# Performance work log

Measured on AMD Instinct MI355X. Metric: run time of the kernel, lower is better.

Reference implementation:

```python
import math
import jax, jax.numpy as jnp
import numpy as np

B, N, D = 16, 2048, 64

def setup_inputs() -> dict:
    key = jax.random.key(0)
    kq, kk, kv, kl = jax.random.split(key, 4)
    q = jax.random.normal(kq, (B, N, D), dtype=jnp.float32)
    k = jax.random.normal(kk, (B, N, D), dtype=jnp.float32)
    v = jax.random.normal(kv, (B, N, D), dtype=jnp.float32)
    valid = jax.random.randint(kl, (B, N), 0, 2048, dtype=jnp.int64 if jax.config.jax_enable_x64 else jnp.int32)
    return {"q": q, "k": k, "v": v, "valid": valid}

def reference(q, k, v, valid):
    # scores[b,i,j] = <q[b,i], k[b,j]> / sqrt(d)
    d = k.shape[-1]
    scores = jnp.einsum('bid,bjd->bij', q, k) / jnp.sqrt(jnp.asarray(d, q.dtype))
    # mask[b,i,j] = (j+1) > valid[b,i]; masked positions replaced by 1e-6
    # (faithful to torch.masked_fill(scores, mask, 1e-06) -- NOT -inf)
    key_pos = jnp.arange(1, scores.shape[-1] + 1)  # [N]
    mask = key_pos[None, None, :] > valid[:, :, None]  # [B,N,N]
    mask_scores = jnp.where(mask, jnp.asarray(1e-06, scores.dtype), scores)
    weights = jax.nn.softmax(mask_scores, axis=-1)
    # dropout p=0.0 -> identity
    return jnp.einsum('bij,bjd->bid', weights, v)
```

## Files before the change

kernel.cpp:

```cpp
#include <hip/hip_runtime.h>
#include <stdint.h>

#define BB 16
#define NN 2048
#define DD 64
#define BM 64
#define BN 64
#define KSTR 72
#define PSTR 72

typedef __attribute__((ext_vector_type(8))) short short8;
typedef __attribute__((ext_vector_type(4))) float f32x4;

__device__ __forceinline__ unsigned short f2bf(float f) {
  union { float f; uint32_t u; } c; c.f = f;
  uint32_t u = c.u + 0x7fffu + ((c.u >> 16) & 1u);
  return (unsigned short)(u >> 16);
}
__device__ __forceinline__ unsigned short f2bf_fast(float f) {
  union { float f; uint32_t u; } c; c.f = f;
  return (unsigned short)((c.u + 0x8000u) >> 16);
}

__global__ __launch_bounds__(256) void prep_kernel(const float* __restrict__ k,
                                                   const float* __restrict__ v,
                                                   unsigned short* __restrict__ kbf,
                                                   unsigned short* __restrict__ vt) {
  __shared__ float t[64][65];
  int id = blockIdx.x, tid = threadIdx.x;
  if (id < 2048) {
    int i = id * 256 + tid;
    float4 f = ((const float4*)k)[i];
    ushort4 o;
    o.x = f2bf(f.x); o.y = f2bf(f.y); o.z = f2bf(f.z); o.w = f2bf(f.w);
    ((ushort4*)kbf)[i] = o;
  } else {
    int bid = id - 2048;
    int b = bid >> 5;
    int k0 = (bid & 31) * 64;
    const float4* src = (const float4*)(v + ((size_t)b * NN + k0) * DD);
#pragma unroll
    for (int i = 0; i < 4; i++) {
      int f4 = tid + i * 256;
      int row = f4 >> 4, c4 = f4 & 15;
      float4 f = src[f4];
      t[row][c4*4+0] = f.x; t[row][c4*4+1] = f.y; t[row][c4*4+2] = f.z; t[row][c4*4+3] = f.w;
    }
    __syncthreads();
    int d = tid >> 2, kg = tid & 3;
    unsigned short* dst = vt + ((size_t)b * DD + d) * NN + k0 + kg * 16;
#pragma unroll
    for (int u = 0; u < 4; u++) {
      ushort4 o;
      o.x = f2bf(t[kg*16+u*4+0][d]);
      o.y = f2bf(t[kg*16+u*4+1][d]);
      o.z = f2bf(t[kg*16+u*4+2][d]);
      o.w = f2bf(t[kg*16+u*4+3][d]);
      ((ushort4*)dst)[u] = o;
    }
  }
}

__global__ __launch_bounds__(256, 4) void attn_kernel(
    const float* __restrict__ q, const unsigned short* __restrict__ kbf,
    const unsigned short* __restrict__ vtbf, const int* __restrict__ valid,
    float* __restrict__ out, unsigned short* __restrict__ po,
    float* __restrict__ pz, int nsplit)
{
  __shared__ __align__(16) unsigned short Klds[BN * KSTR];
  __shared__ __align__(16) unsigned short Vlds[DD * KSTR];
  __shared__ __align__(16) unsigned short Plds[4 * 16 * PSTR];
  __shared__ int vld[BM];

  int id = blockIdx.x;
  int x = id & 7, r = id >> 3;
  int b = x + 8 * (r & 1);
  int r2 = r >> 1;
  int sp, qt;
  if (nsplit == 2) { sp = r2 & 1; qt = r2 >> 1; }
  else             { sp = 0;      qt = r2;      }
  int i0 = qt * BM;
  int jbase = sp * (NN / nsplit);
  int jlen  = NN / nsplit;

  int tid = threadIdx.x;
  int w = tid >> 6;
  int lane = tid & 63;
  int m = lane & 15;
  int quad = lane >> 4;

  if (tid < BM) vld[tid] = valid[b * NN + i0 + tid];

  short8 qf[2];
  {
    const float* qp = q + ((size_t)b * NN + (i0 + w * 16 + m)) * DD;
#pragma unroll
    for (int s = 0; s < 2; s++) {
      float4 f0 = *(const float4*)(qp + s * 32 + quad * 8);
      float4 f1 = *(const float4*)(qp + s * 32 + quad * 8 + 4);
      union { short8 v; unsigned short u[8]; } tmp;
      tmp.u[0]=f2bf(f0.x*0.125f); tmp.u[1]=f2bf(f0.y*0.125f);
      tmp.u[2]=f2bf(f0.z*0.125f); tmp.u[3]=f2bf(f0.w*0.125f);
      tmp.u[4]=f2bf(f1.x*0.125f); tmp.u[5]=f2bf(f1.y*0.125f);
      tmp.u[6]=f2bf(f1.z*0.125f); tmp.u[7]=f2bf(f1.w*0.125f);
      qf[s] = tmp.v;
    }
  }

  __syncthreads();
  int vr[4];
#pragma unroll
  for (int rr = 0; rr < 4; rr++) vr[rr] = vld[w * 16 + quad * 4 + rr];

  f32x4 o[4] = {{0,0,0,0},{0,0,0,0},{0,0,0,0},{0,0,0,0}};
  float z[4] = {0,0,0,0};
  unsigned short* pbase = Plds + w * 16 * PSTR;

  int srow = tid >> 2, scol = (tid & 3) * 16;
  const unsigned short* gk = kbf + ((size_t)(b * NN + jbase + srow)) * DD + scol;
  const unsigned short* gv = vtbf + ((size_t)b * DD + srow) * NN + jbase + scol;

  uint4 ka = *(const uint4*)gk, kb2 = *(const uint4*)(gk + 8);
  uint4 va = *(const uint4*)gv, vb2 = *(const uint4*)(gv + 8);

  int iters = jlen / BN;
  for (int it = 0; it < iters; ++it) {
    int j0 = jbase + it * BN;
    __syncthreads();
    *(uint4*)&Klds[srow * KSTR + scol]     = ka;
    *(uint4*)&Klds[srow * KSTR + scol + 8] = kb2;
    *(uint4*)&Vlds[srow * KSTR + scol]     = va;
    *(uint4*)&Vlds[srow * KSTR + scol + 8] = vb2;
    if (it + 1 < iters) {
      gk += BN * DD; gv += BN;
      ka = *(const uint4*)gk; kb2 = *(const uint4*)(gk + 8);
      va = *(const uint4*)gv; vb2 = *(const uint4*)(gv + 8);
    }
    __syncthreads();

    f32x4 s[4] = {{0,0,0,0},{0,0,0,0},{0,0,0,0},{0,0,0,0}};
#pragma unroll
    for (int sub = 0; sub < 4; sub++) {
#pragma unroll
      for (int ss = 0; ss < 2; ss++) {
        short8 kf = *(const short8*)&Klds[(sub * 16 + m) * KSTR + ss * 32 + quad * 8];
        s[sub] = __builtin_amdgcn_mfma_f32_16x16x32_bf16(qf[ss], kf, s[sub], 0, 0, 0);
      }
    }

#pragma unroll
    for (int sub = 0; sub < 4; sub++) {
      int j = j0 + sub * 16 + m;
#pragma unroll
      for (int rr = 0; rr < 4; rr++) {
        float arg = (j < vr[rr]) ? s[sub][rr] : 1.0e-6f;
        float e = __expf(arg);
        z[rr] += e;
        pbase[(quad * 4 + rr) * PSTR + sub * 16 + m] = f2bf_fast(e);
      }
    }

    __builtin_amdgcn_s_waitcnt(0xc07f);

#pragma unroll
    for (int ss = 0; ss < 2; ss++) {
      short8 pf = *(const short8*)&pbase[m * PSTR + ss * 32 + quad * 8];
#pragma unroll
      for (int t = 0; t < 4; t++) {
        short8 vf = *(const short8*)&Vlds[(t * 16 + m) * KSTR + ss * 32 + quad * 8];
        o[t] = __builtin_amdgcn_mfma_f32_16x16x32_bf16(pf, vf, o[t], 0, 0, 0);
      }
    }
  }

  float zred[4];
#pragma unroll
  for (int rr = 0; rr < 4; rr++) {
    float zz = z[rr];
    zz += __shfl_xor(zz, 1, 16);
    zz += __shfl_xor(zz, 2, 16);
    zz += __shfl_xor(zz, 4, 16);
    zz += __shfl_xor(zz, 8, 16);
    zred[rr] = zz;
  }

  if (nsplit == 2) {
#pragma unroll
    for (int rr = 0; rr < 4; rr++) {
      int row = i0 + w * 16 + quad * 4 + rr;
      unsigned short* op = po + ((size_t)((sp * BB + b) * NN) + row) * DD + m;
#pragma unroll
      for (int t = 0; t < 4; t++) op[t * 16] = f2bf_fast(o[t][rr]);
      if (m == 0) pz[(size_t)(sp * BB + b) * NN + row] = zred[rr];
    }
  } else {
#pragma unroll
    for (int rr = 0; rr < 4; rr++) {
      float inv = 1.0f / zred[rr];
      int row = i0 + w * 16 + quad * 4 + rr;
      float* op = out + ((size_t)b * NN + row) * DD + m;
#pragma unroll
      for (int t = 0; t < 4; t++) op[t * 16] = o[t][rr] * inv;
    }
  }
}

__global__ __launch_bounds__(256) void combine_kernel(const unsigned short* __restrict__ po,
                                                      const float* __restrict__ pz,
                                                      float* __restrict__ out) {
  int gid = blockIdx.x * 256 + threadIdx.x;
  size_t base = (size_t)gid * 8;
  int rowz = gid >> 3;
  uint4 a = *(const uint4*)(po + base);
  uint4 c = *(const uint4*)(po + (size_t)BB * NN * DD + base);
  float inv = 1.0f / (pz[rowz] + pz[(size_t)BB * NN + rowz]);
  uint32_t aw[4] = {a.x, a.y, a.z, a.w}, cw[4] = {c.x, c.y, c.z, c.w};
  float r[8];
#pragma unroll
  for (int i = 0; i < 4; i++) {
    float alo = __uint_as_float(aw[i] << 16), ahi = __uint_as_float(aw[i] & 0xffff0000u);
    float clo = __uint_as_float(cw[i] << 16), chi = __uint_as_float(cw[i] & 0xffff0000u);
    r[2*i]   = (alo + clo) * inv;
    r[2*i+1] = (ahi + chi) * inv;
  }
  float4* op = (float4*)(out + base);
  op[0] = make_float4(r[0], r[1], r[2], r[3]);
  op[1] = make_float4(r[4], r[5], r[6], r[7]);
}

extern "C" void kernel_launch(void* const* d_in, const int* in_sizes, int n_in,
                              void* d_out, int out_size, void* d_ws, size_t ws_size,
                              hipStream_t stream) {
  const float* q = (const float*)d_in[0];
  const float* k = (const float*)d_in[1];
  const float* v = (const float*)d_in[2];
  const int* valid = (const int*)d_in[3];
  float* out = (float*)d_out;

  unsigned short* kbf  = (unsigned short*)d_ws;
  unsigned short* vtbf = kbf + (size_t)BB * NN * DD;
  unsigned short* po   = vtbf + (size_t)BB * NN * DD;
  float* pz = (float*)(po + (size_t)2 * BB * NN * DD);

  size_t need = (size_t)4 * BB * NN * DD * 2 + (size_t)2 * BB * NN * 4;
  int nsplit = (ws_size >= need) ? 2 : 1;

  hipLaunchKernelGGL(prep_kernel, dim3(2560), dim3(256), 0, stream, k, v, kbf, vtbf);
  hipLaunchKernelGGL(attn_kernel, dim3(512 * nsplit), dim3(256), 0, stream,
                     q, kbf, vtbf, valid, out, po, pz, nsplit);
  if (nsplit == 2)
    hipLaunchKernelGGL(combine_kernel, dim3(1024), dim3(256), 0, stream, po, pz, out);
}
```

Before: 117.2 us.

## Template split-K attention with 4-way key split and transposed MFMA operands

After: 115.8 us. No clear change (-1.2%).

```diff
diff --git a/kernel.cpp b/kernel.cpp
--- a/kernel.cpp
+++ b/kernel.cpp
@@ -1,4 +1,5 @@
 #include <hip/hip_runtime.h>
+#include <hip/hip_bf16.h>
 #include <stdint.h>
 
 #define BB 16
@@ -17,9 +18,10 @@
   uint32_t u = c.u + 0x7fffu + ((c.u >> 16) & 1u);
   return (unsigned short)(u >> 16);
 }
-__device__ __forceinline__ unsigned short f2bf_fast(float f) {
-  union { float f; uint32_t u; } c; c.f = f;
-  return (unsigned short)((c.u + 0x8000u) >> 16);
+__device__ __forceinline__ uint32_t pkrn(float a, float b) {
+  union { __hip_bfloat162 h; uint32_t u; } c;
+  c.h = __float22bfloat162_rn(make_float2(a, b));
+  return c.u;
 }
 
 __global__ __launch_bounds__(256) void prep_kernel(const float* __restrict__ k,
@@ -61,27 +63,28 @@
   }
 }
 
+template <int NS>
 __global__ __launch_bounds__(256, 4) void attn_kernel(
     const float* __restrict__ q, const unsigned short* __restrict__ kbf,
     const unsigned short* __restrict__ vtbf, const int* __restrict__ valid,
     float* __restrict__ out, unsigned short* __restrict__ po,
-    float* __restrict__ pz, int nsplit)
+    float* __restrict__ pz)
 {
+  constexpr int JLEN = NN / NS;
+  constexpr int ITERS = JLEN / BN;
+
   __shared__ __align__(16) unsigned short Klds[BN * KSTR];
   __shared__ __align__(16) unsigned short Vlds[DD * KSTR];
   __shared__ __align__(16) unsigned short Plds[4 * 16 * PSTR];
   __shared__ int vld[BM];
 
   int id = blockIdx.x;
-  int x = id & 7, r = id >> 3;
-  int b = x + 8 * (r & 1);
-  int r2 = r >> 1;
-  int sp, qt;
-  if (nsplit == 2) { sp = r2 & 1; qt = r2 >> 1; }
-  else             { sp = 0;      qt = r2;      }
+  int b = (id & 7) + 8 * ((id >> 3) & 1);
+  int rest = id >> 4;
+  int sp = rest % NS;
+  int qt = rest / NS;
   int i0 = qt * BM;
-  int jbase = sp * (NN / nsplit);
-  int jlen  = NN / nsplit;
+  int jbase = sp * JLEN;
 
   int tid = threadIdx.x;
   int w = tid >> 6;
@@ -98,22 +101,20 @@
     for (int s = 0; s < 2; s++) {
       float4 f0 = *(const float4*)(qp + s * 32 + quad * 8);
       float4 f1 = *(const float4*)(qp + s * 32 + quad * 8 + 4);
-      union { short8 v; unsigned short u[8]; } tmp;
-      tmp.u[0]=f2bf(f0.x*0.125f); tmp.u[1]=f2bf(f0.y*0.125f);
-      tmp.u[2]=f2bf(f0.z*0.125f); tmp.u[3]=f2bf(f0.w*0.125f);
-      tmp.u[4]=f2bf(f1.x*0.125f); tmp.u[5]=f2bf(f1.y*0.125f);
-      tmp.u[6]=f2bf(f1.z*0.125f); tmp.u[7]=f2bf(f1.w*0.125f);
+      union { short8 v; uint32_t x[4]; } tmp;
+      tmp.x[0] = pkrn(f0.x * 0.125f, f0.y * 0.125f);
+      tmp.x[1] = pkrn(f0.z * 0.125f, f0.w * 0.125f);
+      tmp.x[2] = pkrn(f1.x * 0.125f, f1.y * 0.125f);
+      tmp.x[3] = pkrn(f1.z * 0.125f, f1.w * 0.125f);
       qf[s] = tmp.v;
     }
   }
 
   __syncthreads();
-  int vr[4];
-#pragma unroll
-  for (int rr = 0; rr < 4; rr++) vr[rr] = vld[w * 16 + quad * 4 + rr];
+  int vq = vld[w * 16 + m];
 
   f32x4 o[4] = {{0,0,0,0},{0,0,0,0},{0,0,0,0},{0,0,0,0}};
-  float z[4] = {0,0,0,0};
+  float z = 0.0f;
   unsigned short* pbase = Plds + w * 16 * PSTR;
 
   int srow = tid >> 2, scol = (tid & 3) * 16;
@@ -123,15 +124,14 @@
   uint4 ka = *(const uint4*)gk, kb2 = *(const uint4*)(gk + 8);
   uint4 va = *(const uint4*)gv, vb2 = *(const uint4*)(gv + 8);
 
-  int iters = jlen / BN;
-  for (int it = 0; it < iters; ++it) {
+  for (int it = 0; it < ITERS; ++it) {
     int j0 = jbase + it * BN;
     __syncthreads();
     *(uint4*)&Klds[srow * KSTR + scol]     = ka;
     *(uint4*)&Klds[srow * KSTR + scol + 8] = kb2;
     *(uint4*)&Vlds[srow * KSTR + scol]     = va;
     *(uint4*)&Vlds[srow * KSTR + scol + 8] = vb2;
-    if (it + 1 < iters) {
+    if (it + 1 < ITERS) {
       gk += BN * DD; gv += BN;
       ka = *(const uint4*)gk; kb2 = *(const uint4*)(gk + 8);
       va = *(const uint4*)gv; vb2 = *(const uint4*)(gv + 8);
@@ -140,24 +140,26 @@
 
     f32x4 s[4] = {{0,0,0,0},{0,0,0,0},{0,0,0,0},{0,0,0,0}};
 #pragma unroll
-    for (int sub = 0; sub < 4; sub++) {
+    for (int c = 0; c < 4; c++) {
 #pragma unroll
       for (int ss = 0; ss < 2; ss++) {
-        short8 kf = *(const short8*)&Klds[(sub * 16 + m) * KSTR + ss * 32 + quad * 8];
-        s[sub] = __builtin_amdgcn_mfma_f32_16x16x32_bf16(qf[ss], kf, s[sub], 0, 0, 0);
+        short8 kf = *(const short8*)&Klds[(c * 16 + m) * KSTR + ss * 32 + quad * 8];
+        s[c] = __builtin_amdgcn_mfma_f32_16x16x32_bf16(kf, qf[ss], s[c], 0, 0, 0);
       }
     }
 
 #pragma unroll
-    for (int sub = 0; sub < 4; sub++) {
-      int j = j0 + sub * 16 + m;
+    for (int c = 0; c < 4; c++) {
+      float e[4];
 #pragma unroll
       for (int rr = 0; rr < 4; rr++) {
-        float arg = (j < vr[rr]) ? s[sub][rr] : 1.0e-6f;
-        float e = __expf(arg);
-        z[rr] += e;
-        pbase[(quad * 4 + rr) * PSTR + sub * 16 + m] = f2bf_fast(e);
+        int j = j0 + c * 16 + quad * 4 + rr;
+        float arg = (j < vq) ? s[c][rr] : 1.0e-6f;
+        e[rr] = __expf(arg);
       }
+      z += (e[0] + e[1]) + (e[2] + e[3]);
+      *(uint2*)&pbase[m * PSTR + c * 16 + quad * 4] =
+          make_uint2(pkrn(e[0], e[1]), pkrn(e[2], e[3]));
     }
 
     __builtin_amdgcn_s_waitcnt(0xc07f);
@@ -168,64 +170,57 @@
 #pragma unroll
       for (int t = 0; t < 4; t++) {
         short8 vf = *(const short8*)&Vlds[(t * 16 + m) * KSTR + ss * 32 + quad * 8];
-        o[t] = __builtin_amdgcn_mfma_f32_16x16x32_bf16(pf, vf, o[t], 0, 0, 0);
+        o[t] = __builtin_amdgcn_mfma_f32_16x16x32_bf16(vf, pf, o[t], 0, 0, 0);
       }
     }
   }
 
-  float zred[4];
-#pragma unroll
-  for (int rr = 0; rr < 4; rr++) {
-    float zz = z[rr];
-    zz += __shfl_xor(zz, 1, 16);
-    zz += __shfl_xor(zz, 2, 16);
-    zz += __shfl_xor(zz, 4, 16);
-    zz += __shfl_xor(zz, 8, 16);
-    zred[rr] = zz;
-  }
-
-  if (nsplit == 2) {
-#pragma unroll
-    for (int rr = 0; rr < 4; rr++) {
-      int row = i0 + w * 16 + quad * 4 + rr;
-      unsigned short* op = po + ((size_t)((sp * BB + b) * NN) + row) * DD + m;
-#pragma unroll
-      for (int t = 0; t < 4; t++) op[t * 16] = f2bf_fast(o[t][rr]);
-      if (m == 0) pz[(size_t)(sp * BB + b) * NN + row] = zred[rr];
-    }
+  z += __shfl_xor(z, 16);
+  z += __shfl_xor(z, 32);
+
+  if (NS > 1) {
+    int row = i0 + w * 16 + m;
+    unsigned short* op = po + ((size_t)((sp * BB + b) * NN) + row) * DD;
+#pragma unroll
+    for (int t = 0; t < 4; t++)
+      *(uint2*)&op[t * 16 + quad * 4] = make_uint2(pkrn(o[t][0], o[t][1]),
+                                                   pkrn(o[t][2], o[t][3]));
+    if (quad == 0) pz[(size_t)(sp * BB + b) * NN + row] = z;
   } else {
-#pragma unroll
-    for (int rr = 0; rr < 4; rr++) {
-      float inv = 1.0f / zred[rr];
-      int row = i0 + w * 16 + quad * 4 + rr;
-      float* op = out + ((size_t)b * NN + row) * DD + m;
-#pragma unroll
-      for (int t = 0; t < 4; t++) op[t * 16] = o[t][rr] * inv;
-    }
-  }
-}
-
+    float inv = 1.0f / z;
+    int row = i0 + w * 16 + m;
+    float* op = out + ((size_t)b * NN + row) * DD;
+#pragma unroll
+    for (int t = 0; t < 4; t++)
+      *(float4*)&op[t * 16 + quad * 4] =
+          make_float4(o[t][0]*inv, o[t][1]*inv, o[t][2]*inv, o[t][3]*inv);
+  }
+}
+
+template <int NS>
 __global__ __launch_bounds__(256) void combine_kernel(const unsigned short* __restrict__ po,
                                                       const float* __restrict__ pz,
                                                       float* __restrict__ out) {
   int gid = blockIdx.x * 256 + threadIdx.x;
   size_t base = (size_t)gid * 8;
   int rowz = gid >> 3;
-  uint4 a = *(const uint4*)(po + base);
-  uint4 c = *(const uint4*)(po + (size_t)BB * NN * DD + base);
-  float inv = 1.0f / (pz[rowz] + pz[(size_t)BB * NN + rowz]);
-  uint32_t aw[4] = {a.x, a.y, a.z, a.w}, cw[4] = {c.x, c.y, c.z, c.w};
-  float r[8];
-#pragma unroll
-  for (int i = 0; i < 4; i++) {
-    float alo = __uint_as_float(aw[i] << 16), ahi = __uint_as_float(aw[i] & 0xffff0000u);
-    float clo = __uint_as_float(cw[i] << 16), chi = __uint_as_float(cw[i] & 0xffff0000u);
-    r[2*i]   = (alo + clo) * inv;
-    r[2*i+1] = (ahi + chi) * inv;
-  }
+  float r[8] = {0,0,0,0,0,0,0,0};
+  float zs = 0.0f;
+#pragma unroll
+  for (int sp = 0; sp < NS; sp++) {
+    uint4 a = *(const uint4*)(po + (size_t)sp * BB * NN * DD + base);
+    zs += pz[(size_t)sp * BB * NN + rowz];
+    uint32_t aw[4] = {a.x, a.y, a.z, a.w};
+#pragma unroll
+    for (int i = 0; i < 4; i++) {
+      r[2*i]   += __uint_as_float(aw[i] << 16);
+      r[2*i+1] += __uint_as_float(aw[i] & 0xffff0000u);
+    }
+  }
+  float inv = 1.0f / zs;
   float4* op = (float4*)(out + base);
-  op[0] = make_float4(r[0], r[1], r[2], r[3]);
-  op[1] = make_float4(r[4], r[5], r[6], r[7]);
+  op[0] = make_float4(r[0]*inv, r[1]*inv, r[2]*inv, r[3]*inv);
+  op[1] = make_float4(r[4]*inv, r[5]*inv, r[6]*inv, r[7]*inv);
 }
 
 extern "C" void kernel_launch(void* const* d_in, const int* in_sizes, int n_in,
@@ -240,14 +235,24 @@
   unsigned short* kbf  = (unsigned short*)d_ws;
   unsigned short* vtbf = kbf + (size_t)BB * NN * DD;
   unsigned short* po   = vtbf + (size_t)BB * NN * DD;
-  float* pz = (float*)(po + (size_t)2 * BB * NN * DD);
-
-  size_t need = (size_t)4 * BB * NN * DD * 2 + (size_t)2 * BB * NN * 4;
-  int nsplit = (ws_size >= need) ? 2 : 1;
+  float* pz4 = (float*)(po + (size_t)4 * BB * NN * DD);
+  float* pz2 = (float*)(po + (size_t)2 * BB * NN * DD);
+
+  size_t fixed = (size_t)2 * BB * NN * DD * 2;
+  size_t need4 = fixed + (size_t)4 * BB * NN * DD * 2 + (size_t)4 * BB * NN * 4;
+  size_t need2 = fixed + (size_t)2 * BB * NN * DD * 2 + (size_t)2 * BB * NN * 4;
 
   hipLaunchKernelGGL(prep_kernel, dim3(2560), dim3(256), 0, stream, k, v, kbf, vtbf);
-  hipLaunchKernelGGL(attn_kernel, dim3(512 * nsplit), dim3(256), 0, stream,
-                     q, kbf, vtbf, valid, out, po, pz, nsplit);
-  if (nsplit == 2)
-    hipLaunchKernelGGL(combine_kernel, dim3(1024), dim3(256), 0, stream, po, pz, out);
-}
+  if (ws_size >= need4) {
+    hipLaunchKernelGGL((attn_kernel<4>), dim3(16 * 32 * 4), dim3(256), 0, stream,
+                       q, kbf, vtbf, valid, out, po, pz4);
+    hipLaunchKernelGGL((combine_kernel<4>), dim3(1024), dim3(256), 0, stream, po, pz4, out);
+  } else if (ws_size >= need2) {
+    hipLaunchKernelGGL((attn_kernel<2>), dim3(16 * 32 * 2), dim3(256), 0, stream,
+                       q, kbf, vtbf, valid, out, po, pz2);
+    hipLaunchKernelGGL((combine_kernel<2>), dim3(1024), dim3(256), 0, stream, po, pz2, out);
+  } else {
+    hipLaunchKernelGGL((attn_kernel<1>), dim3(16 * 32), dim3(256), 0, stream,
+                       q, kbf, vtbf, valid, out, po, pz2);
+  }
+}
```
